# Kernel optimization log

Measured on AMD Instinct MI355X. Metric: run time of the kernel, lower is better.

Reference implementation:

```python
import jax, jax.numpy as jnp
import numpy as np
from jax import lax

SCORE_THRESH = 0.05
NMS_THRESH = 0.5
DET_PER_IMG = 100
K_PRE = 2048  # pre-NMS candidate cap (batched_nms is never run on N*C dense candidates)
BBOX_XFORM_CLIP = float(np.log(1000.0 / 16.0))
WX, WY, WW, WH = 10.0, 10.0, 5.0, 5.0


def _decode(reg, props):
    # reg: [N, C, 4] deltas, props: [N, 4] xyxy -> [N, C, 4] xyxy (torchvision BoxCoder.decode)
    w = props[:, 2] - props[:, 0]
    h = props[:, 3] - props[:, 1]
    cx = props[:, 0] + 0.5 * w
    cy = props[:, 1] + 0.5 * h
    dx = reg[..., 0] / WX
    dy = reg[..., 1] / WY
    dw = jnp.minimum(reg[..., 2] / WW, BBOX_XFORM_CLIP)
    dh = jnp.minimum(reg[..., 3] / WH, BBOX_XFORM_CLIP)
    pcx = dx * w[:, None] + cx[:, None]
    pcy = dy * h[:, None] + cy[:, None]
    pw = jnp.exp(dw) * w[:, None]
    ph = jnp.exp(dh) * h[:, None]
    return jnp.stack([pcx - 0.5 * pw, pcy - 0.5 * ph, pcx + 0.5 * pw, pcy + 0.5 * ph], axis=-1)


def _pairwise_iou(b):
    # b: [K, 4] -> [K, K]
    area = (b[:, 2] - b[:, 0]) * (b[:, 3] - b[:, 1])
    lt = jnp.maximum(b[:, None, :2], b[None, :, :2])
    rb = jnp.minimum(b[:, None, 2:], b[None, :, 2:])
    wh = jnp.clip(rb - lt, 0.0)
    inter = wh[..., 0] * wh[..., 1]
    return inter / (area[:, None] + area[None, :] - inter)


def _greedy_nms(iou, valid, thresh):
    # boxes assumed sorted by descending score; valid: [K] bool initial keep mask
    K = iou.shape[0]
    idx = jnp.arange(K)
    def body(i, keep):
        sup = (iou[i] > thresh) & (idx > i) & keep[i]
        return keep & (~sup)
    return lax.fori_loop(0, K, body, valid)


def _process_image(logits, reg, props, img_h, img_w):
    # logits: [N, C], reg: [N, 4C], props: [N, 4]
    N, C = logits.shape
    scores = jax.nn.softmax(logits, axis=-1)[:, 1:]          # [N, C-1] drop background
    boxes = _decode(reg.reshape(N, C, 4), props)[:, 1:]      # [N, C-1, 4]
    boxes = jnp.stack([
        jnp.clip(boxes[..., 0], 0.0, img_w),
        jnp.clip(boxes[..., 1], 0.0, img_h),
        jnp.clip(boxes[..., 2], 0.0, img_w),
        jnp.clip(boxes[..., 3], 0.0, img_h),
    ], axis=-1)
    labels = jnp.broadcast_to(jnp.arange(1, C), (N, C - 1))
    boxes = boxes.reshape(-1, 4)       # [M, 4], M = N*(C-1)
    scores = scores.reshape(-1)
    labels = labels.reshape(-1)
    wd = boxes[:, 2] - boxes[:, 0]
    ht = boxes[:, 3] - boxes[:, 1]
    valid = (scores > SCORE_THRESH) & (wd >= 1.0) & (ht >= 1.0)  # score thresh + remove_small_boxes
    masked = jnp.where(valid, scores, -1.0)
    top_s, top_i = lax.top_k(masked, K_PRE)
    tb = boxes[top_i]
    tl = labels[top_i]
    tvalid = top_s > SCORE_THRESH
    # batched_nms via per-class coordinate offsets
    off = tl.astype(tb.dtype) * (jnp.max(tb) + 1.0)
    keep = _greedy_nms(_pairwise_iou(tb + off[:, None]), tvalid, NMS_THRESH)
    ks = jnp.where(keep, top_s, -1.0)
    fs, fi = lax.top_k(ks, DET_PER_IMG)
    fvalid = fs > SCORE_THRESH
    out_boxes = jnp.where(fvalid[:, None], tb[fi], 0.0)
    out_scores = jnp.where(fvalid, fs, 0.0)
    out_labels = jnp.where(fvalid, tl[fi], -1)
    return out_boxes, out_scores, out_labels


def setup_inputs() -> dict:
    key = jax.random.key(0)
    k1, k2, k3 = jax.random.split(key, 3)
    B, N, C, H, W = 8, 4000, 91, 800, 800
    pts = jax.random.uniform(k1, (B, N, 2, 2), dtype=jnp.float32, minval=0.0, maxval=float(W))
    proposals = jnp.concatenate([pts.min(axis=2), pts.max(axis=2)], axis=-1)  # valid xyxy
    class_logits = jax.random.normal(k2, (B * N, C), dtype=jnp.float32)
    box_regression = 0.5 * jax.random.normal(k3, (B * N, 4 * C), dtype=jnp.float32)
    return {"class_logits": class_logits, "box_regression": box_regression,
            "proposals": proposals, "img_h": H, "img_w": W}


def reference(class_logits, box_regression, proposals, img_h, img_w):
    B, N, _ = proposals.shape
    C = class_logits.shape[-1]
    logits = class_logits.reshape(B, N, C)
    reg = box_regression.reshape(B, N, 4 * C)
    fn = lambda l, r, p: _process_image(l, r, p, float(img_h), float(img_w))
    boxes, scores, labels = jax.vmap(fn)(logits, reg, proposals)
    return boxes, scores, labels
```

## Files before the change

kernel.cpp:

```cpp
#include <hip/hip_runtime.h>
#include <stdint.h>

typedef unsigned int u32;
typedef unsigned long long u64;
typedef __attribute__((ext_vector_type(2))) unsigned long long u64x2;

#define BIMG 8
#define NPROP 4000
#define NCLS 91
#define CM1 90
#define MCAND (NPROP * CM1)
#define KPRE 2048
#define NBUCKET 4096
#define NREP 8
#define SELCAP 16384
#define DETS 100
#define WLCAP 2048
#define SCORE_T 0.05f
#define NMS_T 0.5f
#define BBOX_CLIP 4.135166556742356f

#define HISTREP_OFF ((size_t)0)
#define BCNTREP_OFF (HISTREP_OFF + (size_t)NREP * BIMG * NBUCKET * 4)
#define META_OFF    (BCNTREP_OFF + (size_t)NREP * BIMG * NBUCKET * 4)
#define ZERO_BYTES  (META_OFF + 4096)
#define START_OFF   (ZERO_BYTES)
#define HISTTOT_OFF (START_OFF + (size_t)BIMG * NBUCKET * 4)
#define STARTREP_OFF (HISTTOT_OFF + (size_t)BIMG * NBUCKET * 4)
#define SEL_OFF     (STARTREP_OFF + (size_t)NREP * BIMG * NBUCKET * 4)
#define TBOX_OFF    (SEL_OFF + (size_t)BIMG * SELCAP * 8)
#define TSB_OFF     (TBOX_OFF + (size_t)BIMG * KPRE * 16)
#define TSC_OFF     (TSB_OFF + (size_t)BIMG * KPRE * 16)
#define TLB_OFF     (TSC_OFF + (size_t)BIMG * KPRE * 4)
#define TVL_OFF     (TLB_OFF + (size_t)BIMG * KPRE * 4)
#define KEEP_OFF    (TVL_OFF + (size_t)BIMG * KPRE * 4)
#define WLIST_OFF   (KEEP_OFF + (size_t)BIMG * 32 * 8)
#define UNION_OFF   (WLIST_OFF + (size_t)BIMG * WLCAP * 4)
#define UNION_BYTES ((size_t)BIMG * MCAND * 4)
#define MASK_BYTES  ((size_t)BIMG * KPRE * 32 * 8)
#define WS_NEED     (UNION_OFF + UNION_BYTES)

__device__ __forceinline__ void decode_clip(const float4 rg, const float w, const float h,
                                            const float cx, const float cy,
                                            const float fw, const float fh, float bx[4]) {
    float dx = rg.x / 10.0f;
    float dy = rg.y / 10.0f;
    float dw = fminf(rg.z / 5.0f, BBOX_CLIP);
    float dh = fminf(rg.w / 5.0f, BBOX_CLIP);
    float pcx = dx * w + cx;
    float pcy = dy * h + cy;
    float pw  = expf(dw) * w;
    float phh = expf(dh) * h;
    bx[0] = fminf(fmaxf(pcx - 0.5f * pw,  0.0f), fw);
    bx[1] = fminf(fmaxf(pcy - 0.5f * phh, 0.0f), fh);
    bx[2] = fminf(fmaxf(pcx + 0.5f * pw,  0.0f), fw);
    bx[3] = fminf(fmaxf(pcy + 0.5f * phh, 0.0f), fh);
}

__global__ __launch_bounds__(256) void k1_score_hist(
    const float* __restrict__ logits, const float* __restrict__ reg,
    const float* __restrict__ props, const int* __restrict__ imh, const int* __restrict__ imw,
    u32* __restrict__ histrep, u32* __restrict__ cand_ord) {
    const int lane = threadIdx.x & 63;
    const int pid = blockIdx.x * 4 + (threadIdx.x >> 6);
    if (pid >= BIMG * NPROP) return;
    const int img = pid / NPROP;
    const float fw = (float)imw[0], fh = (float)imh[0];
    const float* lrow = logits + (size_t)pid * NCLS;
    float v0 = lrow[lane];
    float v1 = (lane < 27) ? lrow[lane + 64] : -3.0e38f;
    float mx = fmaxf(v0, v1);
#pragma unroll
    for (int o = 32; o > 0; o >>= 1) mx = fmaxf(mx, __shfl_xor(mx, o));
    float es = expf(v0 - mx) + ((lane < 27) ? expf(v1 - mx) : 0.0f);
#pragma unroll
    for (int o = 32; o > 0; o >>= 1) es += __shfl_xor(es, o);
    const float thr = mx + logf(es) - 2.9967323f;
    float4 p = reinterpret_cast<const float4*>(props)[pid];
    const float w = p.z - p.x, h = p.w - p.y;
    const float cx = p.x + 0.5f * w, cy = p.y + 0.5f * h;
    const float4* rrow = reinterpret_cast<const float4*>(reg) + (size_t)pid * NCLS;
    const int n = pid - img * NPROP;
    u32* co = cand_ord + (size_t)img * MCAND + (size_t)n * CM1;
#pragma unroll
    for (int batch = 0; batch < 2; ++batch) {
        int ci = lane + batch * 64;
        if (ci < CM1) {
            int c = ci + 1;
            float l = lrow[c];
            u32 o = 0u;
            if (l > thr) {
                float sc = expf(l - mx) / es;
                float4 rg = rrow[c];
                float bx[4];
                decode_clip(rg, w, h, cx, cy, fw, fh, bx);
                bool valid = (sc > SCORE_T) && (bx[2] - bx[0] >= 1.0f) && (bx[3] - bx[1] >= 1.0f);
                if (valid) {
                    o = __float_as_uint(sc) | 0x80000000u;
                    u32 t = (u32)img * MCAND + (u32)n * CM1 + (u32)ci;
                    int rep = (int)((t >> 8) & (NREP - 1));
                    atomicAdd(&histrep[((size_t)rep * BIMG + img) * NBUCKET + (o >> 20)], 1u);
                }
            }
            co[ci] = o;
        }
    }
}

__global__ __launch_bounds__(256) void k2_scan(
    const u32* __restrict__ histrep, u32* __restrict__ histtot,
    u32* __restrict__ start, u32* __restrict__ startrep, u32* __restrict__ meta,
    u32* __restrict__ wlist) {
    const int img = blockIdx.x;
    const int td = threadIdx.x;
    const int lane = td & 63, wv = td >> 6;
    u32 cnt[16]; u32 tsum = 0;
#pragma unroll
    for (int k = 0; k < 16; ++k) {
        const int bk = NBUCKET - 1 - (td * 16 + k);
        u32 c = 0;
#pragma unroll
        for (int r = 0; r < NREP; ++r)
            c += histrep[((size_t)r * BIMG + img) * NBUCKET + bk];
        cnt[k] = c; tsum += c;
    }
    u32 inc = tsum;
#pragma unroll
    for (int o = 1; o < 64; o <<= 1) { u32 t = __shfl_up(inc, o); if (lane >= o) inc += t; }
    __shared__ u32 wsum[4];
    __shared__ u32 TbkS, Vs;
    if (td == 0) TbkS = 0u;
    if (lane == 63) wsum[wv] = inc;
    __syncthreads();
    u32 wbase = 0;
    for (int i = 0; i < wv; ++i) wbase += wsum[i];
    if (td == 255) Vs = wbase + inc;
    const u32 excl0 = wbase + inc - tsum;
    u32 excl = excl0;
#pragma unroll
    for (int k = 0; k < 16; ++k) {
        const int bk = NBUCKET - 1 - (td * 16 + k);
        const u32 c = cnt[k];
        start[img * NBUCKET + bk] = excl;
        histtot[img * NBUCKET + bk] = c;
        u32 sub = excl;
#pragma unroll
        for (int r = 0; r < NREP; ++r) {
            startrep[((size_t)r * BIMG + img) * NBUCKET + bk] = sub;
            sub += histrep[((size_t)r * BIMG + img) * NBUCKET + bk];
        }
        if (c > 0 && excl < KPRE && excl + c >= KPRE) TbkS = (u32)bk;
        excl += c;
    }
    u32 qcnt = 0;
    {
        u32 e = excl0;
#pragma unroll
        for (int k = 0; k < 16; ++k) {
            if (cnt[k] >= 2 && e < KPRE) ++qcnt;
            e += cnt[k];
        }
    }
    u32 qinc = qcnt;
#pragma unroll
    for (int o = 1; o < 64; o <<= 1) { u32 t = __shfl_up(qinc, o); if (lane >= o) qinc += t; }
    __shared__ u32 qws[4];
    if (lane == 63) qws[wv] = qinc;
    __syncthreads();
    u32 qbase = 0;
    for (int i = 0; i < wv; ++i) qbase += qws[i];
    u32 qoff = qbase + qinc - qcnt;
    {
        u32 e = excl0;
#pragma unroll
        for (int k = 0; k < 16; ++k) {
            const int bk = NBUCKET - 1 - (td * 16 + k);
            if (cnt[k] >= 2 && e < KPRE && qoff < WLCAP) wlist[img * WLCAP + (qoff++)] = (u32)bk;
            e += cnt[k];
        }
    }
    if (td == 255) meta[img * 8 + 3] = qbase + qinc;
    __syncthreads();
    if (td == 0) {
        u32 V = Vs;
        meta[img * 8 + 0] = V;
        meta[img * 8 + 1] = TbkS;
        meta[img * 8 + 2] = (V < KPRE) ? (KPRE - V) : 0u;
    }
}

__global__ __launch_bounds__(256) void k3_compact(
    const u32* __restrict__ cand_ord, const u32* __restrict__ startrep,
    const u32* __restrict__ meta, u32* __restrict__ bcntrep, u64* __restrict__ sel) {
    const u32 t = blockIdx.x * 256 + threadIdx.x;
    const int rep = (int)(blockIdx.x & (NREP - 1));
    if (t >= (u32)(BIMG * MCAND)) return;
    const int img = t / MCAND;
    const u32 idx = t - (u32)img * MCAND;
    const u32 o = cand_ord[t];
    if (!o) return;
    const u32 bk = o >> 20;
    if (bk < meta[img * 8 + 1]) return;
    const size_t ri = ((size_t)rep * BIMG + img) * NBUCKET + bk;
    const u32 pos = startrep[ri] + atomicAdd(&bcntrep[ri], 1u);
    if (pos < SELCAP)
        sel[(size_t)img * SELCAP + pos] = ((u64)o << 32) | (u32)(~idx);
}

__global__ __launch_bounds__(64) void k3b_fill(
    const u32* __restrict__ cand_ord, const u32* __restrict__ meta, u64* __restrict__ sel) {
    const int img = blockIdx.x;
    const u32 need = meta[img * 8 + 2];
    if (need == 0) return;
    const u32 V = meta[img * 8 + 0];
    const int lane = threadIdx.x;
    const u32 ORDN1 = 0x407FFFFFu;
    u32 filled = 0;
    for (u32 b0 = 0; b0 < MCAND && filled < need; b0 += 64) {
        u32 idx = b0 + lane;
        bool inv = (idx < MCAND) && (cand_ord[(size_t)img * MCAND + idx] == 0u);
        u64 bal = __ballot(inv);
        u32 pre = (u32)__popcll(bal & ((1ull << lane) - 1ull));
        if (inv && (filled + pre) < need)
            sel[(size_t)img * SELCAP + V + filled + pre] = ((u64)ORDN1 << 32) | (u32)(~idx);
        filled += (u32)__popcll(bal);
    }
}

__global__ __launch_bounds__(256) void k4_sortseg(
    const u32* __restrict__ histtot, const u32* __restrict__ start,
    const u32* __restrict__ meta, const u32* __restrict__ wlist, u64* __restrict__ sel) {
    __shared__ u64 arr[4096];
    const int img = blockIdx.y;
    const int tid = threadIdx.x;
    const u32 wcount = meta[img * 8 + 3];
    for (u32 wi = blockIdx.x; wi < wcount; wi += gridDim.x) {
        const u32 bk = (wi < WLCAP) ? wlist[img * WLCAP + wi] : 0u;
        u32 cnt = histtot[img * NBUCKET + bk];
        u32 st = start[img * NBUCKET + bk];
        if (cnt < 2 || st >= KPRE) continue;
        if (st + cnt > SELCAP) cnt = SELCAP - st;
        if (cnt > 4096) cnt = 4096;
        int n = 1;
        while (n < (int)cnt) n <<= 1;
        u64* seg = sel + (size_t)img * SELCAP + st;
        for (int i = tid; i < n; i += 256) arr[i] = (i < (int)cnt) ? seg[i] : 0ull;
        __syncthreads();
        for (int k = 2; k <= n; k <<= 1)
            for (int j = k >> 1; j > 0; j >>= 1) {
                for (int i = tid; i < n; i += 256) {
                    int ixj = i ^ j;
                    if (ixj > i) {
                        u64 a = arr[i], b = arr[ixj];
                        bool swp = ((i & k) == 0) ? (a < b) : (a > b);
                        if (swp) { arr[i] = b; arr[ixj] = a; }
                    }
                }
                __syncthreads();
            }
        for (int i = tid; i < (int)cnt; i += 256) seg[i] = arr[i];
        __syncthreads();
    }
}

__global__ __launch_bounds__(256) void k5_gather(
    const u64* __restrict__ sel, const float* __restrict__ reg, const float* __restrict__ props,
    const int* __restrict__ imh, const int* __restrict__ imw,
    float* __restrict__ tbox, float* __restrict__ tsb, float* __restrict__ tsc,
    int* __restrict__ tlb, u32* __restrict__ tvl) {
    const int img = blockIdx.x;
    const int tid = threadIdx.x;
    const float fw = (float)imw[0], fh = (float)imh[0];
    float bx[8][4];
    int lab[8];
    float lm = -3.0e38f;
#pragma unroll
    for (int t = 0; t < 8; ++t) {
        int s = t * 256 + tid;
        u64 key = sel[(size_t)img * SELCAP + s];
        u32 o = (u32)(key >> 32);
        u32 idx = ~((u32)key);
        u32 b = (o & 0x80000000u) ? (o & 0x7FFFFFFFu) : ~o;
        float sc = __uint_as_float(b);
        u32 n = idx / CM1;
        int c = (int)(idx - n * CM1) + 1;
        int pid = img * NPROP + (int)n;
        float4 p = reinterpret_cast<const float4*>(props)[pid];
        float w = p.z - p.x, h = p.w - p.y;
        float cx = p.x + 0.5f * w, cy = p.y + 0.5f * h;
        float4 rg = reinterpret_cast<const float4*>(reg)[(size_t)pid * NCLS + c];
        decode_clip(rg, w, h, cx, cy, fw, fh, bx[t]);
        lab[t] = c;
        lm = fmaxf(lm, fmaxf(fmaxf(bx[t][0], bx[t][1]), fmaxf(bx[t][2], bx[t][3])));
        reinterpret_cast<float4*>(tbox)[(size_t)img * KPRE + s] =
            make_float4(bx[t][0], bx[t][1], bx[t][2], bx[t][3]);
        tsc[(size_t)img * KPRE + s] = sc;
        tlb[(size_t)img * KPRE + s] = c;
        tvl[(size_t)img * KPRE + s] = (sc > SCORE_T) ? 1u : 0u;
    }
#pragma unroll
    for (int o2 = 32; o2 > 0; o2 >>= 1) lm = fmaxf(lm, __shfl_xor(lm, o2));
    __shared__ float wm[4];
    if ((tid & 63) == 0) wm[tid >> 6] = lm;
    __syncthreads();
    float mplus = fmaxf(fmaxf(wm[0], wm[1]), fmaxf(wm[2], wm[3])) + 1.0f;
#pragma unroll
    for (int t = 0; t < 8; ++t) {
        int s = t * 256 + tid;
        float off = (float)lab[t] * mplus;
        reinterpret_cast<float4*>(tsb)[(size_t)img * KPRE + s] =
            make_float4(bx[t][0] + off, bx[t][1] + off, bx[t][2] + off, bx[t][3] + off);
    }
}

__global__ __launch_bounds__(64) void k6_mask(
    const float* __restrict__ tsb, u64* __restrict__ mask) {
    if (blockIdx.x < blockIdx.y) return;
    const int img = blockIdx.z;
    const int j0 = blockIdx.x * 64;
    const int i0 = blockIdx.y * 64;
    const int tid = threadIdx.x;
    __shared__ float4 cb[64];
    __shared__ float ca[64];
    float4 c = reinterpret_cast<const float4*>(tsb)[(size_t)img * KPRE + j0 + tid];
    cb[tid] = c;
    ca[tid] = (c.z - c.x) * (c.w - c.y);
    __syncthreads();
    const int i = i0 + tid;
    float4 r = reinterpret_cast<const float4*>(tsb)[(size_t)img * KPRE + i];
    float ra = (r.z - r.x) * (r.w - r.y);
    u64 bits = 0ull;
#pragma unroll 8
    for (int jj = 0; jj < 64; ++jj) {
        int j = j0 + jj;
        float4 cc = cb[jj];
        float wv = fmaxf(fminf(r.z, cc.z) - fmaxf(r.x, cc.x), 0.0f);
        float hv = fmaxf(fminf(r.w, cc.w) - fmaxf(r.y, cc.y), 0.0f);
        float inter = wv * hv;
        float iou = inter / ((ra + ca[jj]) - inter);
        if ((iou > NMS_T) && (j > i)) bits |= (1ull << jj);
    }
    mask[((size_t)img * KPRE + i) * 32 + (j0 >> 6)] = bits;
}

__device__ __forceinline__ u64 rdlane64(u64 v, int l) {
    u32 lo = (u32)__builtin_amdgcn_readlane((int)(u32)v, l);
    u32 hi = (u32)__builtin_amdgcn_readlane((int)(u32)(v >> 32), l);
    return ((u64)hi << 32) | lo;
}

__device__ __forceinline__ void g2l16(const void* g, void* l) {
    __builtin_amdgcn_global_load_lds(
        (const __attribute__((address_space(1))) void*)g,
        (__attribute__((address_space(3))) void*)l, 16, 0, 0);
}

__global__ __launch_bounds__(64) void k7_nms(
    const u64* __restrict__ mask, const u32* __restrict__ tvl, u64* __restrict__ keepw) {
    __shared__ u64 lbuf[2][2048];
    const int img = blockIdx.x;
    const int lane = threadIdx.x;
    const int lg = lane >> 4;
    const u64* mrow = mask + (size_t)img * KPRE * 32;

    u64 accx = 0ull, accy = 0ull, rp = 0ull;
    for (int w = 0; w < 32; ++w) {
        bool tv = tvl[(size_t)img * KPRE + w * 64 + lane] != 0u;
        u64 iw = ~__ballot(tv);
        if (w == 0) rp = iw;
        if ((lane & 15) == (w >> 1)) { if (w & 1) accy = iw; else accx = iw; }
    }

    {
        const char* gsrc = (const char*)mrow + (size_t)lane * 16;
#pragma unroll
        for (int t = 0; t < 16; ++t)
            g2l16(gsrc + (size_t)t * 1024, (char*)&lbuf[0][0] + (size_t)t * 1024);
    }
    u64 diag = mrow[(size_t)lane * 32];

    u32 tk = 0;
    int bcut = 31;

#pragma unroll 1
    for (int b = 0; b < 32; ++b) {
        const size_t base32 = (size_t)b * 2048;
        const u64* cbuf = &lbuf[b & 1][0];

        u64 diagn = 0ull;
        if (b + 1 < 32) {
            diagn = mrow[base32 + 2048 + (size_t)lane * 32 + (b + 1)];
            const char* gsrc = (const char*)(mrow + base32 + 2048) + (size_t)lane * 16;
            char* nb_l = (char*)&lbuf[(b + 1) & 1][0];
#pragma unroll
            for (int t = 0; t < 16; ++t)
                g2l16(gsrc + (size_t)t * 1024, nb_l + (size_t)t * 1024);
        }

        u64 A = rp;
#pragma unroll
        for (int u = 0; u < 64; ++u) {
            u64 row = rdlane64(diag, u);
            if (!((A >> u) & 1ull)) A |= row;
        }
        const u64 keptw = ~A;

        if (b + 1 < 32) asm volatile("s_waitcnt vmcnt(17)" ::: "memory");
        else            asm volatile("s_waitcnt vmcnt(0)" ::: "memory");

#define LDV(K) u64x2 v##K = *(const u64x2*)&cbuf[128 * (K) + 2 * lane];
#define PRV(K) { u32 nib = (u32)(keptw >> (4 * (K))) & 15u; \
                 u32 kb = (nib >> lg) & 1u; \
                 accx |= kb ? v##K.x : 0ull; accy |= kb ? v##K.y : 0ull; }
        LDV(0) LDV(1) LDV(2) LDV(3)
        LDV(4) LDV(5) LDV(6) LDV(7)     PRV(0) PRV(1) PRV(2) PRV(3)
        LDV(8) LDV(9) LDV(10) LDV(11)   PRV(4) PRV(5) PRV(6) PRV(7)
        LDV(12) LDV(13) LDV(14) LDV(15) PRV(8) PRV(9) PRV(10) PRV(11)
        PRV(12) PRV(13) PRV(14) PRV(15)
#undef LDV
#undef PRV

        tk += (u32)__popcll(keptw);
        if (tk >= (u32)DETS) { bcut = b; break; }

        const int nb2 = b + 1;
        if (nb2 < 32) {
            u64 asel = (nb2 & 1) ? accy : accx;
            const int sl = (nb2 >> 1) & 15;
            rp = rdlane64(asel, sl) | rdlane64(asel, sl + 16) |
                 rdlane64(asel, sl + 32) | rdlane64(asel, sl + 48);
        }
        diag = diagn;
    }

    asm volatile("s_waitcnt vmcnt(0)" ::: "memory");

    accx |= __shfl_xor(accx, 16); accx |= __shfl_xor(accx, 32);
    accy |= __shfl_xor(accy, 16); accy |= __shfl_xor(accy, 32);
    if (lane < 16) {
        keepw[img * 32 + 2 * lane]     = (2 * lane     <= bcut) ? ~accx : 0ull;
        keepw[img * 32 + 2 * lane + 1] = (2 * lane + 1 <= bcut) ? ~accy : 0ull;
    }
}

__global__ __launch_bounds__(64) void k8_select(
    const u64* __restrict__ keepw, const float* __restrict__ tsc,
    const float* __restrict__ tbox, const int* __restrict__ tlb,
    float* __restrict__ out) {
    const int img = blockIdx.x;
    const int lane = threadIdx.x;
    u64 kw = (lane < 32) ? keepw[img * 32 + lane] : 0ull;
    u32 cnt = (u32)__popcll(kw);
    u32 inc = cnt;
#pragma unroll
    for (int o = 1; o < 64; o <<= 1) { u32 t = __shfl_up(inc, o); if (lane >= o) inc += t; }
    const u32 excl = inc - cnt;
    const u32 total = (u32)__shfl(inc, 63);

    float* ob0 = out + (size_t)img * DETS * 4;
    float* os0 = out + (size_t)BIMG * DETS * 4 + (size_t)img * DETS;
    float* ol0 = out + (size_t)BIMG * DETS * 5 + (size_t)img * DETS;

#pragma unroll
    for (int t = 0; t < 2; ++t) {
        u32 r = (u32)lane + (u32)t * 64;
        if (r < DETS && r >= total) {
            reinterpret_cast<float4*>(ob0)[r] = make_float4(0.f, 0.f, 0.f, 0.f);
            os0[r] = 0.0f;
            ol0[r] = -1.0f;
        }
    }

    u64 w = kw;
    u32 r = excl;
    while (w != 0ull && r < DETS) {
        int p = __ffsll((unsigned long long)w) - 1;
        w &= (w - 1ull);
        u32 s = (u32)lane * 64u + (u32)p;
        reinterpret_cast<float4*>(ob0)[r] =
            reinterpret_cast<const float4*>(tbox)[(size_t)img * KPRE + s];
        os0[r] = tsc[(size_t)img * KPRE + s];
        ol0[r] = (float)tlb[(size_t)img * KPRE + s];
        ++r;
    }
}

extern "C" void kernel_launch(void* const* d_in, const int* in_sizes, int n_in,
                              void* d_out, int out_size, void* d_ws, size_t ws_size,
                              hipStream_t stream) {
    const float* logits = (const float*)d_in[0];
    const float* reg    = (const float*)d_in[1];
    const float* props  = (const float*)d_in[2];
    const int*   imh    = (const int*)d_in[3];
    const int*   imw    = (const int*)d_in[4];
    float* out = (float*)d_out;
    char* ws = (char*)d_ws;
    if (ws_size < WS_NEED) return;

    u32* histrep  = (u32*)(ws + HISTREP_OFF);
    u32* bcntrep  = (u32*)(ws + BCNTREP_OFF);
    u32* meta     = (u32*)(ws + META_OFF);
    u32* start    = (u32*)(ws + START_OFF);
    u32* histtot  = (u32*)(ws + HISTTOT_OFF);
    u32* startrep = (u32*)(ws + STARTREP_OFF);
    u64* sel  = (u64*)(ws + SEL_OFF);
    float* tbox = (float*)(ws + TBOX_OFF);
    float* tsb  = (float*)(ws + TSB_OFF);
    float* tsc  = (float*)(ws + TSC_OFF);
    int*   tlb  = (int*)(ws + TLB_OFF);
    u32*   tvl  = (u32*)(ws + TVL_OFF);
    u64*   keepw = (u64*)(ws + KEEP_OFF);
    u32*   wlist = (u32*)(ws + WLIST_OFF);
    u32*   cand_ord = (u32*)(ws + UNION_OFF);
    u64*   mask = (u64*)(ws + UNION_OFF);

    hipMemsetAsync(d_ws, 0, ZERO_BYTES, stream);

    k1_score_hist<<<BIMG * NPROP / 4, 256, 0, stream>>>(logits, reg, props, imh, imw,
                                                        histrep, cand_ord);
    k2_scan<<<BIMG, 256, 0, stream>>>(histrep, histtot, start, startrep, meta, wlist);
    k3_compact<<<(BIMG * MCAND) / 256, 256, 0, stream>>>(cand_ord, startrep, meta, bcntrep, sel);
    k3b_fill<<<BIMG, 64, 0, stream>>>(cand_ord, meta, sel);
    hipMemsetAsync(mask, 0, MASK_BYTES, stream);
    k4_sortseg<<<dim3(64, BIMG), 256, 0, stream>>>(histtot, start, meta, wlist, sel);
    k5_gather<<<BIMG, 256, 0, stream>>>(sel, reg, props, imh, imw, tbox, tsb, tsc, tlb, tvl);
    k6_mask<<<dim3(32, 32, BIMG), 64, 0, stream>>>(tsb, mask);
    k7_nms<<<BIMG, 64, 0, stream>>>(mask, tvl, keepw);
    k8_select<<<BIMG, 64, 0, stream>>>(keepw, tsc, tbox, tlb, out);
}
```

Baseline: 272.8 us.

## Fuse all pipeline stages into one cooperative persistent kernel with grid syncs

Replaces the ten separate launches (two memsets plus eight kernels) with a single cooperative kernel of 256 blocks. Stages are separated by grid.sync(), workspace zeroing moves into the kernel, and the NMS and selection stages are merged so the keep words never round-trip through memory. This aims to remove per-launch overhead and inter-kernel gaps. In exchange, stages that used many blocks now run with a fixed 65536 threads, and each grid barrier has its own cost.

New measurement: 494.4 us. 81.3% more time.

```diff
diff --git a/kernel.cpp b/kernel.cpp
--- a/kernel.cpp
+++ b/kernel.cpp
@@ -1,5 +1,8 @@
 #include <hip/hip_runtime.h>
+#include <hip/hip_cooperative_groups.h>
 #include <stdint.h>
+
+namespace cg = cooperative_groups;
 
 typedef unsigned int u32;
 typedef unsigned long long u64;
@@ -37,8 +40,11 @@
 #define WLIST_OFF   (KEEP_OFF + (size_t)BIMG * 32 * 8)
 #define UNION_OFF   (WLIST_OFF + (size_t)BIMG * WLCAP * 4)
 #define UNION_BYTES ((size_t)BIMG * MCAND * 4)
-#define MASK_BYTES  ((size_t)BIMG * KPRE * 32 * 8)
 #define WS_NEED     (UNION_OFF + UNION_BYTES)
+
+#define ZW ((u32)(ZERO_BYTES / 4))
+#define MW ((u32)(BIMG * KPRE * 32))
+#define NTHREADS 65536
 
 __device__ __forceinline__ void decode_clip(const float4 rg, const float w, const float h,
                                             const float cx, const float cy,
@@ -57,292 +63,6 @@
     bx[3] = fminf(fmaxf(pcy + 0.5f * phh, 0.0f), fh);
 }
 
-__global__ __launch_bounds__(256) void k1_score_hist(
-    const float* __restrict__ logits, const float* __restrict__ reg,
-    const float* __restrict__ props, const int* __restrict__ imh, const int* __restrict__ imw,
-    u32* __restrict__ histrep, u32* __restrict__ cand_ord) {
-    const int lane = threadIdx.x & 63;
-    const int pid = blockIdx.x * 4 + (threadIdx.x >> 6);
-    if (pid >= BIMG * NPROP) return;
-    const int img = pid / NPROP;
-    const float fw = (float)imw[0], fh = (float)imh[0];
-    const float* lrow = logits + (size_t)pid * NCLS;
-    float v0 = lrow[lane];
-    float v1 = (lane < 27) ? lrow[lane + 64] : -3.0e38f;
-    float mx = fmaxf(v0, v1);
-#pragma unroll
-    for (int o = 32; o > 0; o >>= 1) mx = fmaxf(mx, __shfl_xor(mx, o));
-    float es = expf(v0 - mx) + ((lane < 27) ? expf(v1 - mx) : 0.0f);
-#pragma unroll
-    for (int o = 32; o > 0; o >>= 1) es += __shfl_xor(es, o);
-    const float thr = mx + logf(es) - 2.9967323f;
-    float4 p = reinterpret_cast<const float4*>(props)[pid];
-    const float w = p.z - p.x, h = p.w - p.y;
-    const float cx = p.x + 0.5f * w, cy = p.y + 0.5f * h;
-    const float4* rrow = reinterpret_cast<const float4*>(reg) + (size_t)pid * NCLS;
-    const int n = pid - img * NPROP;
-    u32* co = cand_ord + (size_t)img * MCAND + (size_t)n * CM1;
-#pragma unroll
-    for (int batch = 0; batch < 2; ++batch) {
-        int ci = lane + batch * 64;
-        if (ci < CM1) {
-            int c = ci + 1;
-            float l = lrow[c];
-            u32 o = 0u;
-            if (l > thr) {
-                float sc = expf(l - mx) / es;
-                float4 rg = rrow[c];
-                float bx[4];
-                decode_clip(rg, w, h, cx, cy, fw, fh, bx);
-                bool valid = (sc > SCORE_T) && (bx[2] - bx[0] >= 1.0f) && (bx[3] - bx[1] >= 1.0f);
-                if (valid) {
-                    o = __float_as_uint(sc) | 0x80000000u;
-                    u32 t = (u32)img * MCAND + (u32)n * CM1 + (u32)ci;
-                    int rep = (int)((t >> 8) & (NREP - 1));
-                    atomicAdd(&histrep[((size_t)rep * BIMG + img) * NBUCKET + (o >> 20)], 1u);
-                }
-            }
-            co[ci] = o;
-        }
-    }
-}
-
-__global__ __launch_bounds__(256) void k2_scan(
-    const u32* __restrict__ histrep, u32* __restrict__ histtot,
-    u32* __restrict__ start, u32* __restrict__ startrep, u32* __restrict__ meta,
-    u32* __restrict__ wlist) {
-    const int img = blockIdx.x;
-    const int td = threadIdx.x;
-    const int lane = td & 63, wv = td >> 6;
-    u32 cnt[16]; u32 tsum = 0;
-#pragma unroll
-    for (int k = 0; k < 16; ++k) {
-        const int bk = NBUCKET - 1 - (td * 16 + k);
-        u32 c = 0;
-#pragma unroll
-        for (int r = 0; r < NREP; ++r)
-            c += histrep[((size_t)r * BIMG + img) * NBUCKET + bk];
-        cnt[k] = c; tsum += c;
-    }
-    u32 inc = tsum;
-#pragma unroll
-    for (int o = 1; o < 64; o <<= 1) { u32 t = __shfl_up(inc, o); if (lane >= o) inc += t; }
-    __shared__ u32 wsum[4];
-    __shared__ u32 TbkS, Vs;
-    if (td == 0) TbkS = 0u;
-    if (lane == 63) wsum[wv] = inc;
-    __syncthreads();
-    u32 wbase = 0;
-    for (int i = 0; i < wv; ++i) wbase += wsum[i];
-    if (td == 255) Vs = wbase + inc;
-    const u32 excl0 = wbase + inc - tsum;
-    u32 excl = excl0;
-#pragma unroll
-    for (int k = 0; k < 16; ++k) {
-        const int bk = NBUCKET - 1 - (td * 16 + k);
-        const u32 c = cnt[k];
-        start[img * NBUCKET + bk] = excl;
-        histtot[img * NBUCKET + bk] = c;
-        u32 sub = excl;
-#pragma unroll
-        for (int r = 0; r < NREP; ++r) {
-            startrep[((size_t)r * BIMG + img) * NBUCKET + bk] = sub;
-            sub += histrep[((size_t)r * BIMG + img) * NBUCKET + bk];
-        }
-        if (c > 0 && excl < KPRE && excl + c >= KPRE) TbkS = (u32)bk;
-        excl += c;
-    }
-    u32 qcnt = 0;
-    {
-        u32 e = excl0;
-#pragma unroll
-        for (int k = 0; k < 16; ++k) {
-            if (cnt[k] >= 2 && e < KPRE) ++qcnt;
-            e += cnt[k];
-        }
-    }
-    u32 qinc = qcnt;
-#pragma unroll
-    for (int o = 1; o < 64; o <<= 1) { u32 t = __shfl_up(qinc, o); if (lane >= o) qinc += t; }
-    __shared__ u32 qws[4];
-    if (lane == 63) qws[wv] = qinc;
-    __syncthreads();
-    u32 qbase = 0;
-    for (int i = 0; i < wv; ++i) qbase += qws[i];
-    u32 qoff = qbase + qinc - qcnt;
-    {
-        u32 e = excl0;
-#pragma unroll
-        for (int k = 0; k < 16; ++k) {
-            const int bk = NBUCKET - 1 - (td * 16 + k);
-            if (cnt[k] >= 2 && e < KPRE && qoff < WLCAP) wlist[img * WLCAP + (qoff++)] = (u32)bk;
-            e += cnt[k];
-        }
-    }
-    if (td == 255) meta[img * 8 + 3] = qbase + qinc;
-    __syncthreads();
-    if (td == 0) {
-        u32 V = Vs;
-        meta[img * 8 + 0] = V;
-        meta[img * 8 + 1] = TbkS;
-        meta[img * 8 + 2] = (V < KPRE) ? (KPRE - V) : 0u;
-    }
-}
-
-__global__ __launch_bounds__(256) void k3_compact(
-    const u32* __restrict__ cand_ord, const u32* __restrict__ startrep,
-    const u32* __restrict__ meta, u32* __restrict__ bcntrep, u64* __restrict__ sel) {
-    const u32 t = blockIdx.x * 256 + threadIdx.x;
-    const int rep = (int)(blockIdx.x & (NREP - 1));
-    if (t >= (u32)(BIMG * MCAND)) return;
-    const int img = t / MCAND;
-    const u32 idx = t - (u32)img * MCAND;
-    const u32 o = cand_ord[t];
-    if (!o) return;
-    const u32 bk = o >> 20;
-    if (bk < meta[img * 8 + 1]) return;
-    const size_t ri = ((size_t)rep * BIMG + img) * NBUCKET + bk;
-    const u32 pos = startrep[ri] + atomicAdd(&bcntrep[ri], 1u);
-    if (pos < SELCAP)
-        sel[(size_t)img * SELCAP + pos] = ((u64)o << 32) | (u32)(~idx);
-}
-
-__global__ __launch_bounds__(64) void k3b_fill(
-    const u32* __restrict__ cand_ord, const u32* __restrict__ meta, u64* __restrict__ sel) {
-    const int img = blockIdx.x;
-    const u32 need = meta[img * 8 + 2];
-    if (need == 0) return;
-    const u32 V = meta[img * 8 + 0];
-    const int lane = threadIdx.x;
-    const u32 ORDN1 = 0x407FFFFFu;
-    u32 filled = 0;
-    for (u32 b0 = 0; b0 < MCAND && filled < need; b0 += 64) {
-        u32 idx = b0 + lane;
-        bool inv = (idx < MCAND) && (cand_ord[(size_t)img * MCAND + idx] == 0u);
-        u64 bal = __ballot(inv);
-        u32 pre = (u32)__popcll(bal & ((1ull << lane) - 1ull));
-        if (inv && (filled + pre) < need)
-            sel[(size_t)img * SELCAP + V + filled + pre] = ((u64)ORDN1 << 32) | (u32)(~idx);
-        filled += (u32)__popcll(bal);
-    }
-}
-
-__global__ __launch_bounds__(256) void k4_sortseg(
-    const u32* __restrict__ histtot, const u32* __restrict__ start,
-    const u32* __restrict__ meta, const u32* __restrict__ wlist, u64* __restrict__ sel) {
-    __shared__ u64 arr[4096];
-    const int img = blockIdx.y;
-    const int tid = threadIdx.x;
-    const u32 wcount = meta[img * 8 + 3];
-    for (u32 wi = blockIdx.x; wi < wcount; wi += gridDim.x) {
-        const u32 bk = (wi < WLCAP) ? wlist[img * WLCAP + wi] : 0u;
-        u32 cnt = histtot[img * NBUCKET + bk];
-        u32 st = start[img * NBUCKET + bk];
-        if (cnt < 2 || st >= KPRE) continue;
-        if (st + cnt > SELCAP) cnt = SELCAP - st;
-        if (cnt > 4096) cnt = 4096;
-        int n = 1;
-        while (n < (int)cnt) n <<= 1;
-        u64* seg = sel + (size_t)img * SELCAP + st;
-        for (int i = tid; i < n; i += 256) arr[i] = (i < (int)cnt) ? seg[i] : 0ull;
-        __syncthreads();
-        for (int k = 2; k <= n; k <<= 1)
-            for (int j = k >> 1; j > 0; j >>= 1) {
-                for (int i = tid; i < n; i += 256) {
-                    int ixj = i ^ j;
-                    if (ixj > i) {
-                        u64 a = arr[i], b = arr[ixj];
-                        bool swp = ((i & k) == 0) ? (a < b) : (a > b);
-                        if (swp) { arr[i] = b; arr[ixj] = a; }
-                    }
-                }
-                __syncthreads();
-            }
-        for (int i = tid; i < (int)cnt; i += 256) seg[i] = arr[i];
-        __syncthreads();
-    }
-}
-
-__global__ __launch_bounds__(256) void k5_gather(
-    const u64* __restrict__ sel, const float* __restrict__ reg, const float* __restrict__ props,
-    const int* __restrict__ imh, const int* __restrict__ imw,
-    float* __restrict__ tbox, float* __restrict__ tsb, float* __restrict__ tsc,
-    int* __restrict__ tlb, u32* __restrict__ tvl) {
-    const int img = blockIdx.x;
-    const int tid = threadIdx.x;
-    const float fw = (float)imw[0], fh = (float)imh[0];
-    float bx[8][4];
-    int lab[8];
-    float lm = -3.0e38f;
-#pragma unroll
-    for (int t = 0; t < 8; ++t) {
-        int s = t * 256 + tid;
-        u64 key = sel[(size_t)img * SELCAP + s];
-        u32 o = (u32)(key >> 32);
-        u32 idx = ~((u32)key);
-        u32 b = (o & 0x80000000u) ? (o & 0x7FFFFFFFu) : ~o;
-        float sc = __uint_as_float(b);
-        u32 n = idx / CM1;
-        int c = (int)(idx - n * CM1) + 1;
-        int pid = img * NPROP + (int)n;
-        float4 p = reinterpret_cast<const float4*>(props)[pid];
-        float w = p.z - p.x, h = p.w - p.y;
-        float cx = p.x + 0.5f * w, cy = p.y + 0.5f * h;
-        float4 rg = reinterpret_cast<const float4*>(reg)[(size_t)pid * NCLS + c];
-        decode_clip(rg, w, h, cx, cy, fw, fh, bx[t]);
-        lab[t] = c;
-        lm = fmaxf(lm, fmaxf(fmaxf(bx[t][0], bx[t][1]), fmaxf(bx[t][2], bx[t][3])));
-        reinterpret_cast<float4*>(tbox)[(size_t)img * KPRE + s] =
-            make_float4(bx[t][0], bx[t][1], bx[t][2], bx[t][3]);
-        tsc[(size_t)img * KPRE + s] = sc;
-        tlb[(size_t)img * KPRE + s] = c;
-        tvl[(size_t)img * KPRE + s] = (sc > SCORE_T) ? 1u : 0u;
-    }
-#pragma unroll
-    for (int o2 = 32; o2 > 0; o2 >>= 1) lm = fmaxf(lm, __shfl_xor(lm, o2));
-    __shared__ float wm[4];
-    if ((tid & 63) == 0) wm[tid >> 6] = lm;
-    __syncthreads();
-    float mplus = fmaxf(fmaxf(wm[0], wm[1]), fmaxf(wm[2], wm[3])) + 1.0f;
-#pragma unroll
-    for (int t = 0; t < 8; ++t) {
-        int s = t * 256 + tid;
-        float off = (float)lab[t] * mplus;
-        reinterpret_cast<float4*>(tsb)[(size_t)img * KPRE + s] =
-            make_float4(bx[t][0] + off, bx[t][1] + off, bx[t][2] + off, bx[t][3] + off);
-    }
-}
-
-__global__ __launch_bounds__(64) void k6_mask(
-    const float* __restrict__ tsb, u64* __restrict__ mask) {
-    if (blockIdx.x < blockIdx.y) return;
-    const int img = blockIdx.z;
-    const int j0 = blockIdx.x * 64;
-    const int i0 = blockIdx.y * 64;
-    const int tid = threadIdx.x;
-    __shared__ float4 cb[64];
-    __shared__ float ca[64];
-    float4 c = reinterpret_cast<const float4*>(tsb)[(size_t)img * KPRE + j0 + tid];
-    cb[tid] = c;
-    ca[tid] = (c.z - c.x) * (c.w - c.y);
-    __syncthreads();
-    const int i = i0 + tid;
-    float4 r = reinterpret_cast<const float4*>(tsb)[(size_t)img * KPRE + i];
-    float ra = (r.z - r.x) * (r.w - r.y);
-    u64 bits = 0ull;
-#pragma unroll 8
-    for (int jj = 0; jj < 64; ++jj) {
-        int j = j0 + jj;
-        float4 cc = cb[jj];
-        float wv = fmaxf(fminf(r.z, cc.z) - fmaxf(r.x, cc.x), 0.0f);
-        float hv = fmaxf(fminf(r.w, cc.w) - fmaxf(r.y, cc.y), 0.0f);
-        float inter = wv * hv;
-        float iou = inter / ((ra + ca[jj]) - inter);
-        if ((iou > NMS_T) && (j > i)) bits |= (1ull << jj);
-    }
-    mask[((size_t)img * KPRE + i) * 32 + (j0 >> 6)] = bits;
-}
-
 __device__ __forceinline__ u64 rdlane64(u64 v, int l) {
     u32 lo = (u32)__builtin_amdgcn_readlane((int)(u32)v, l);
     u32 hi = (u32)__builtin_amdgcn_readlane((int)(u32)(v >> 32), l);
@@ -355,133 +75,419 @@
         (__attribute__((address_space(3))) void*)l, 16, 0, 0);
 }
 
-__global__ __launch_bounds__(64) void k7_nms(
-    const u64* __restrict__ mask, const u32* __restrict__ tvl, u64* __restrict__ keepw) {
-    __shared__ u64 lbuf[2][2048];
-    const int img = blockIdx.x;
-    const int lane = threadIdx.x;
-    const int lg = lane >> 4;
-    const u64* mrow = mask + (size_t)img * KPRE * 32;
-
-    u64 accx = 0ull, accy = 0ull, rp = 0ull;
-    for (int w = 0; w < 32; ++w) {
-        bool tv = tvl[(size_t)img * KPRE + w * 64 + lane] != 0u;
-        u64 iw = ~__ballot(tv);
-        if (w == 0) rp = iw;
-        if ((lane & 15) == (w >> 1)) { if (w & 1) accy = iw; else accx = iw; }
-    }
+__global__ __launch_bounds__(256) void mega(
+    const float* __restrict__ logits, const float* __restrict__ reg,
+    const float* __restrict__ props, const int* __restrict__ imh,
+    const int* __restrict__ imw,
+    u32* __restrict__ histrep, u32* __restrict__ bcntrep, u32* __restrict__ meta,
+    u32* __restrict__ start, u32* __restrict__ histtot, u32* __restrict__ startrep,
+    u64* __restrict__ sel, float* __restrict__ tbox, float* __restrict__ tsb,
+    float* __restrict__ tsc, int* __restrict__ tlb, u32* __restrict__ tvl,
+    u32* __restrict__ wlist, u32* cand_ord, u64* mask,
+    float* __restrict__ out) {
+    cg::grid_group grid = cg::this_grid();
+    __shared__ u64 smem[4096];
+    __shared__ u32 s_wsum[4], s_qws[4], s_TbkS, s_Vs;
+    __shared__ float s_wm[4];
+
+    const int tid = threadIdx.x;
+    const u32 gtid = blockIdx.x * 256u + (u32)tid;
+    const int lane = tid & 63;
+
+    for (u32 i = gtid; i < ZW; i += NTHREADS) histrep[i] = 0u;
+    grid.sync();
 
     {
-        const char* gsrc = (const char*)mrow + (size_t)lane * 16;
-#pragma unroll
-        for (int t = 0; t < 16; ++t)
-            g2l16(gsrc + (size_t)t * 1024, (char*)&lbuf[0][0] + (size_t)t * 1024);
-    }
-    u64 diag = mrow[(size_t)lane * 32];
-
-    u32 tk = 0;
-    int bcut = 31;
+        const int wid = (int)(gtid >> 6);
+        const float fw = (float)imw[0], fh = (float)imh[0];
+        for (int pid = wid; pid < BIMG * NPROP; pid += NTHREADS / 64) {
+            const int img = pid / NPROP;
+            const float* lrow = logits + (size_t)pid * NCLS;
+            float v0 = lrow[lane];
+            float v1 = (lane < 27) ? lrow[lane + 64] : -3.0e38f;
+            float mx = fmaxf(v0, v1);
+#pragma unroll
+            for (int o = 32; o > 0; o >>= 1) mx = fmaxf(mx, __shfl_xor(mx, o));
+            float es = expf(v0 - mx) + ((lane < 27) ? expf(v1 - mx) : 0.0f);
+#pragma unroll
+            for (int o = 32; o > 0; o >>= 1) es += __shfl_xor(es, o);
+            const float thr = mx + logf(es) - 2.9967323f;
+            float4 p = reinterpret_cast<const float4*>(props)[pid];
+            const float w = p.z - p.x, h = p.w - p.y;
+            const float cx = p.x + 0.5f * w, cy = p.y + 0.5f * h;
+            const float4* rrow = reinterpret_cast<const float4*>(reg) + (size_t)pid * NCLS;
+            const int n = pid - img * NPROP;
+            u32* co = cand_ord + (size_t)img * MCAND + (size_t)n * CM1;
+#pragma unroll
+            for (int batch = 0; batch < 2; ++batch) {
+                int ci = lane + batch * 64;
+                if (ci < CM1) {
+                    int c = ci + 1;
+                    float l = lrow[c];
+                    u32 o = 0u;
+                    if (l > thr) {
+                        float sc = expf(l - mx) / es;
+                        float4 rg = rrow[c];
+                        float bx[4];
+                        decode_clip(rg, w, h, cx, cy, fw, fh, bx);
+                        bool valid = (sc > SCORE_T) && (bx[2] - bx[0] >= 1.0f) &&
+                                     (bx[3] - bx[1] >= 1.0f);
+                        if (valid) {
+                            o = __float_as_uint(sc) | 0x80000000u;
+                            u32 t = (u32)img * MCAND + (u32)n * CM1 + (u32)ci;
+                            int rep = (int)((t >> 8) & (NREP - 1));
+                            atomicAdd(&histrep[((size_t)rep * BIMG + img) * NBUCKET + (o >> 20)], 1u);
+                        }
+                    }
+                    co[ci] = o;
+                }
+            }
+        }
+    }
+    grid.sync();
+
+    if (blockIdx.x < BIMG) {
+        const int img = blockIdx.x;
+        const int td = tid;
+        const int wv = td >> 6;
+        u32 cnt[16]; u32 tsum = 0;
+#pragma unroll
+        for (int k = 0; k < 16; ++k) {
+            const int bk = NBUCKET - 1 - (td * 16 + k);
+            u32 c = 0;
+#pragma unroll
+            for (int r = 0; r < NREP; ++r)
+                c += histrep[((size_t)r * BIMG + img) * NBUCKET + bk];
+            cnt[k] = c; tsum += c;
+        }
+        u32 inc = tsum;
+#pragma unroll
+        for (int o = 1; o < 64; o <<= 1) { u32 t = __shfl_up(inc, o); if (lane >= o) inc += t; }
+        if (td == 0) s_TbkS = 0u;
+        if (lane == 63) s_wsum[wv] = inc;
+        __syncthreads();
+        u32 wbase = 0;
+        for (int i = 0; i < wv; ++i) wbase += s_wsum[i];
+        if (td == 255) s_Vs = wbase + inc;
+        const u32 excl0 = wbase + inc - tsum;
+        u32 excl = excl0;
+#pragma unroll
+        for (int k = 0; k < 16; ++k) {
+            const int bk = NBUCKET - 1 - (td * 16 + k);
+            const u32 c = cnt[k];
+            start[img * NBUCKET + bk] = excl;
+            histtot[img * NBUCKET + bk] = c;
+            u32 sub = excl;
+#pragma unroll
+            for (int r = 0; r < NREP; ++r) {
+                startrep[((size_t)r * BIMG + img) * NBUCKET + bk] = sub;
+                sub += histrep[((size_t)r * BIMG + img) * NBUCKET + bk];
+            }
+            if (c > 0 && excl < KPRE && excl + c >= KPRE) s_TbkS = (u32)bk;
+            excl += c;
+        }
+        u32 qcnt = 0;
+        {
+            u32 e = excl0;
+#pragma unroll
+            for (int k = 0; k < 16; ++k) { if (cnt[k] >= 2 && e < KPRE) ++qcnt; e += cnt[k]; }
+        }
+        u32 qinc = qcnt;
+#pragma unroll
+        for (int o = 1; o < 64; o <<= 1) { u32 t = __shfl_up(qinc, o); if (lane >= o) qinc += t; }
+        if (lane == 63) s_qws[wv] = qinc;
+        __syncthreads();
+        u32 qbase = 0;
+        for (int i = 0; i < wv; ++i) qbase += s_qws[i];
+        u32 qoff = qbase + qinc - qcnt;
+        {
+            u32 e = excl0;
+#pragma unroll
+            for (int k = 0; k < 16; ++k) {
+                const int bk = NBUCKET - 1 - (td * 16 + k);
+                if (cnt[k] >= 2 && e < KPRE && qoff < WLCAP) wlist[img * WLCAP + (qoff++)] = (u32)bk;
+                e += cnt[k];
+            }
+        }
+        if (td == 255) meta[img * 8 + 3] = qbase + qinc;
+        __syncthreads();
+        if (td == 0) {
+            u32 V = s_Vs;
+            meta[img * 8 + 0] = V;
+            meta[img * 8 + 1] = s_TbkS;
+            meta[img * 8 + 2] = (V < KPRE) ? (KPRE - V) : 0u;
+        }
+    }
+    grid.sync();
+
+    {
+        const u32 TOT = (u32)BIMG * (u32)MCAND;
+        for (u32 t = gtid; t < TOT; t += NTHREADS) {
+            const u32 o = cand_ord[t];
+            if (!o) continue;
+            const int img = (int)(t / (u32)MCAND);
+            const u32 idx = t - (u32)img * (u32)MCAND;
+            const u32 bk = o >> 20;
+            if (bk < meta[img * 8 + 1]) continue;
+            const int rep = (int)((t >> 8) & (NREP - 1));
+            const size_t ri = ((size_t)rep * BIMG + img) * NBUCKET + bk;
+            const u32 pos = startrep[ri] + atomicAdd(&bcntrep[ri], 1u);
+            if (pos < SELCAP)
+                sel[(size_t)img * SELCAP + pos] = ((u64)o << 32) | (u32)(~idx);
+        }
+        if (blockIdx.x < BIMG && tid < 64) {
+            const int img = blockIdx.x;
+            const u32 need = meta[img * 8 + 2];
+            if (need != 0) {
+                const u32 V = meta[img * 8 + 0];
+                const u32 ORDN1 = 0x407FFFFFu;
+                u32 filled = 0;
+                for (u32 b0 = 0; b0 < MCAND && filled < need; b0 += 64) {
+                    u32 idx = b0 + (u32)lane;
+                    bool inv = (idx < MCAND) && (cand_ord[(size_t)img * MCAND + idx] == 0u);
+                    u64 bal = __ballot(inv);
+                    u32 pre = (u32)__popcll(bal & ((1ull << lane) - 1ull));
+                    if (inv && (filled + pre) < need)
+                        sel[(size_t)img * SELCAP + V + filled + pre] =
+                            ((u64)ORDN1 << 32) | (u32)(~idx);
+                    filled += (u32)__popcll(bal);
+                }
+            }
+        }
+    }
+    grid.sync();
+
+    {
+        for (u32 i = gtid; i < MW; i += NTHREADS) mask[i] = 0ull;
+
+        const int img = blockIdx.x & 7;
+        const u32 wcount = meta[img * 8 + 3];
+        u64* arr = smem;
+        for (u32 wi = (u32)(blockIdx.x >> 3); wi < wcount; wi += 32) {
+            const u32 bk = (wi < WLCAP) ? wlist[img * WLCAP + wi] : 0u;
+            u32 cnt = histtot[img * NBUCKET + bk];
+            u32 st = start[img * NBUCKET + bk];
+            if (cnt < 2 || st >= KPRE) continue;
+            if (st + cnt > SELCAP) cnt = SELCAP - st;
+            if (cnt > 4096) cnt = 4096;
+            int n = 1;
+            while (n < (int)cnt) n <<= 1;
+            u64* seg = sel + (size_t)img * SELCAP + st;
+            for (int i = tid; i < n; i += 256) arr[i] = (i < (int)cnt) ? seg[i] : 0ull;
+            __syncthreads();
+            for (int k = 2; k <= n; k <<= 1)
+                for (int j = k >> 1; j > 0; j >>= 1) {
+                    for (int i = tid; i < n; i += 256) {
+                        int ixj = i ^ j;
+                        if (ixj > i) {
+                            u64 a = arr[i], b = arr[ixj];
+                            bool swp = ((i & k) == 0) ? (a < b) : (a > b);
+                            if (swp) { arr[i] = b; arr[ixj] = a; }
+                        }
+                    }
+                    __syncthreads();
+                }
+            for (int i = tid; i < (int)cnt; i += 256) seg[i] = arr[i];
+            __syncthreads();
+        }
+    }
+    grid.sync();
+
+    if (blockIdx.x < BIMG) {
+        const int img = blockIdx.x;
+        const float fw = (float)imw[0], fh = (float)imh[0];
+        float bx[8][4];
+        int lab[8];
+        float lm = -3.0e38f;
+#pragma unroll
+        for (int t = 0; t < 8; ++t) {
+            int s = t * 256 + tid;
+            u64 key = sel[(size_t)img * SELCAP + s];
+            u32 o = (u32)(key >> 32);
+            u32 idx = ~((u32)key);
+            u32 b = (o & 0x80000000u) ? (o & 0x7FFFFFFFu) : ~o;
+            float sc = __uint_as_float(b);
+            u32 n = idx / CM1;
+            int c = (int)(idx - n * CM1) + 1;
+            int pid = img * NPROP + (int)n;
+            float4 p = reinterpret_cast<const float4*>(props)[pid];
+            float w = p.z - p.x, h = p.w - p.y;
+            float cx = p.x + 0.5f * w, cy = p.y + 0.5f * h;
+            float4 rg = reinterpret_cast<const float4*>(reg)[(size_t)pid * NCLS + c];
+            decode_clip(rg, w, h, cx, cy, fw, fh, bx[t]);
+            lab[t] = c;
+            lm = fmaxf(lm, fmaxf(fmaxf(bx[t][0], bx[t][1]), fmaxf(bx[t][2], bx[t][3])));
+            reinterpret_cast<float4*>(tbox)[(size_t)img * KPRE + s] =
+                make_float4(bx[t][0], bx[t][1], bx[t][2], bx[t][3]);
+            tsc[(size_t)img * KPRE + s] = sc;
+            tlb[(size_t)img * KPRE + s] = c;
+            tvl[(size_t)img * KPRE + s] = (sc > SCORE_T) ? 1u : 0u;
+        }
+#pragma unroll
+        for (int o2 = 32; o2 > 0; o2 >>= 1) lm = fmaxf(lm, __shfl_xor(lm, o2));
+        if (lane == 0) s_wm[tid >> 6] = lm;
+        __syncthreads();
+        float mplus = fmaxf(fmaxf(s_wm[0], s_wm[1]), fmaxf(s_wm[2], s_wm[3])) + 1.0f;
+#pragma unroll
+        for (int t = 0; t < 8; ++t) {
+            int s = t * 256 + tid;
+            float off = (float)lab[t] * mplus;
+            reinterpret_cast<float4*>(tsb)[(size_t)img * KPRE + s] =
+                make_float4(bx[t][0] + off, bx[t][1] + off, bx[t][2] + off, bx[t][3] + off);
+        }
+    }
+    grid.sync();
+
+    {
+        const int wid = (int)(gtid >> 6);
+        for (int T = wid; T < BIMG * 528; T += NTHREADS / 64) {
+            const int img = T / 528;
+            int rem = T - img * 528;
+            int by = 0;
+            while (rem >= 32 - by) { rem -= (32 - by); ++by; }
+            const int bx_ = by + rem;
+            const int i0 = by * 64, j0 = bx_ * 64;
+            const float4* tsb4 = reinterpret_cast<const float4*>(tsb) + (size_t)img * KPRE;
+            float4 c = tsb4[j0 + lane];
+            float cao = (c.z - c.x) * (c.w - c.y);
+            float4 r = tsb4[i0 + lane];
+            float ra = (r.z - r.x) * (r.w - r.y);
+            const int i = i0 + lane;
+            u64 bits = 0ull;
+#pragma unroll 8
+            for (int jj = 0; jj < 64; ++jj) {
+                float ccx = __shfl(c.x, jj), ccy = __shfl(c.y, jj);
+                float ccz = __shfl(c.z, jj), ccw = __shfl(c.w, jj);
+                float caj = __shfl(cao, jj);
+                float wv = fmaxf(fminf(r.z, ccz) - fmaxf(r.x, ccx), 0.0f);
+                float hv = fmaxf(fminf(r.w, ccw) - fmaxf(r.y, ccy), 0.0f);
+                float inter = wv * hv;
+                float iou = inter / ((ra + caj) - inter);
+                int j = j0 + jj;
+                if ((iou > NMS_T) && (j > i)) bits |= (1ull << jj);
+            }
+            mask[((size_t)img * KPRE + i) * 32 + (j0 >> 6)] = bits;
+        }
+    }
+    grid.sync();
+
+    if (blockIdx.x < BIMG && tid < 64) {
+        const int img = blockIdx.x;
+        const int lg = lane >> 4;
+        const u64* mrow = mask + (size_t)img * KPRE * 32;
+
+        u64 accx = 0ull, accy = 0ull, rp = 0ull;
+        for (int w = 0; w < 32; ++w) {
+            bool tv = tvl[(size_t)img * KPRE + w * 64 + lane] != 0u;
+            u64 iw = ~__ballot(tv);
+            if (w == 0) rp = iw;
+            if ((lane & 15) == (w >> 1)) { if (w & 1) accy = iw; else accx = iw; }
+        }
+
+        {
+            const char* gsrc = (const char*)mrow + (size_t)lane * 16;
+#pragma unroll
+            for (int t = 0; t < 16; ++t)
+                g2l16(gsrc + (size_t)t * 1024, (char*)smem + (size_t)t * 1024);
+        }
+        u64 diag = mrow[(size_t)lane * 32];
+
+        u32 tk = 0;
+        int bcut = 31;
 
 #pragma unroll 1
-    for (int b = 0; b < 32; ++b) {
-        const size_t base32 = (size_t)b * 2048;
-        const u64* cbuf = &lbuf[b & 1][0];
-
-        u64 diagn = 0ull;
-        if (b + 1 < 32) {
-            diagn = mrow[base32 + 2048 + (size_t)lane * 32 + (b + 1)];
-            const char* gsrc = (const char*)(mrow + base32 + 2048) + (size_t)lane * 16;
-            char* nb_l = (char*)&lbuf[(b + 1) & 1][0];
-#pragma unroll
-            for (int t = 0; t < 16; ++t)
-                g2l16(gsrc + (size_t)t * 1024, nb_l + (size_t)t * 1024);
-        }
-
-        u64 A = rp;
-#pragma unroll
-        for (int u = 0; u < 64; ++u) {
-            u64 row = rdlane64(diag, u);
-            if (!((A >> u) & 1ull)) A |= row;
-        }
-        const u64 keptw = ~A;
-
-        if (b + 1 < 32) asm volatile("s_waitcnt vmcnt(17)" ::: "memory");
-        else            asm volatile("s_waitcnt vmcnt(0)" ::: "memory");
+        for (int b = 0; b < 32; ++b) {
+            const size_t base32 = (size_t)b * 2048;
+            const u64* cbuf = smem + (size_t)(b & 1) * 2048;
+
+            u64 diagn = 0ull;
+            if (b + 1 < 32) {
+                diagn = mrow[base32 + 2048 + (size_t)lane * 32 + (b + 1)];
+                const char* gsrc = (const char*)(mrow + base32 + 2048) + (size_t)lane * 16;
+                char* nb_l = (char*)(smem + (size_t)((b + 1) & 1) * 2048);
+#pragma unroll
+                for (int t = 0; t < 16; ++t)
+                    g2l16(gsrc + (size_t)t * 1024, nb_l + (size_t)t * 1024);
+            }
+
+            u64 A = rp;
+#pragma unroll
+            for (int u = 0; u < 64; ++u) {
+                u64 row = rdlane64(diag, u);
+                if (!((A >> u) & 1ull)) A |= row;
+            }
+            const u64 keptw = ~A;
+
+            if (b + 1 < 32) asm volatile("s_waitcnt vmcnt(17)" ::: "memory");
+            else            asm volatile("s_waitcnt vmcnt(0)" ::: "memory");
 
 #define LDV(K) u64x2 v##K = *(const u64x2*)&cbuf[128 * (K) + 2 * lane];
 #define PRV(K) { u32 nib = (u32)(keptw >> (4 * (K))) & 15u; \
                  u32 kb = (nib >> lg) & 1u; \
                  accx |= kb ? v##K.x : 0ull; accy |= kb ? v##K.y : 0ull; }
-        LDV(0) LDV(1) LDV(2) LDV(3)
-        LDV(4) LDV(5) LDV(6) LDV(7)     PRV(0) PRV(1) PRV(2) PRV(3)
-        LDV(8) LDV(9) LDV(10) LDV(11)   PRV(4) PRV(5) PRV(6) PRV(7)
-        LDV(12) LDV(13) LDV(14) LDV(15) PRV(8) PRV(9) PRV(10) PRV(11)
-        PRV(12) PRV(13) PRV(14) PRV(15)
+            LDV(0) LDV(1) LDV(2) LDV(3)
+            LDV(4) LDV(5) LDV(6) LDV(7)     PRV(0) PRV(1) PRV(2) PRV(3)
+            LDV(8) LDV(9) LDV(10) LDV(11)   PRV(4) PRV(5) PRV(6) PRV(7)
+            LDV(12) LDV(13) LDV(14) LDV(15) PRV(8) PRV(9) PRV(10) PRV(11)
+            PRV(12) PRV(13) PRV(14) PRV(15)
 #undef LDV
 #undef PRV
 
-        tk += (u32)__popcll(keptw);
-        if (tk >= (u32)DETS) { bcut = b; break; }
-
-        const int nb2 = b + 1;
-        if (nb2 < 32) {
-            u64 asel = (nb2 & 1) ? accy : accx;
-            const int sl = (nb2 >> 1) & 15;
-            rp = rdlane64(asel, sl) | rdlane64(asel, sl + 16) |
-                 rdlane64(asel, sl + 32) | rdlane64(asel, sl + 48);
-        }
-        diag = diagn;
-    }
-
-    asm volatile("s_waitcnt vmcnt(0)" ::: "memory");
-
-    accx |= __shfl_xor(accx, 16); accx |= __shfl_xor(accx, 32);
-    accy |= __shfl_xor(accy, 16); accy |= __shfl_xor(accy, 32);
-    if (lane < 16) {
-        keepw[img * 32 + 2 * lane]     = (2 * lane     <= bcut) ? ~accx : 0ull;
-        keepw[img * 32 + 2 * lane + 1] = (2 * lane + 1 <= bcut) ? ~accy : 0ull;
-    }
-}
-
-__global__ __launch_bounds__(64) void k8_select(
-    const u64* __restrict__ keepw, const float* __restrict__ tsc,
-    const float* __restrict__ tbox, const int* __restrict__ tlb,
-    float* __restrict__ out) {
-    const int img = blockIdx.x;
-    const int lane = threadIdx.x;
-    u64 kw = (lane < 32) ? keepw[img * 32 + lane] : 0ull;
-    u32 cnt = (u32)__popcll(kw);
-    u32 inc = cnt;
-#pragma unroll
-    for (int o = 1; o < 64; o <<= 1) { u32 t = __shfl_up(inc, o); if (lane >= o) inc += t; }
-    const u32 excl = inc - cnt;
-    const u32 total = (u32)__shfl(inc, 63);
-
-    float* ob0 = out + (size_t)img * DETS * 4;
-    float* os0 = out + (size_t)BIMG * DETS * 4 + (size_t)img * DETS;
-    float* ol0 = out + (size_t)BIMG * DETS * 5 + (size_t)img * DETS;
-
-#pragma unroll
-    for (int t = 0; t < 2; ++t) {
-        u32 r = (u32)lane + (u32)t * 64;
-        if (r < DETS && r >= total) {
-            reinterpret_cast<float4*>(ob0)[r] = make_float4(0.f, 0.f, 0.f, 0.f);
-            os0[r] = 0.0f;
-            ol0[r] = -1.0f;
-        }
-    }
-
-    u64 w = kw;
-    u32 r = excl;
-    while (w != 0ull && r < DETS) {
-        int p = __ffsll((unsigned long long)w) - 1;
-        w &= (w - 1ull);
-        u32 s = (u32)lane * 64u + (u32)p;
-        reinterpret_cast<float4*>(ob0)[r] =
-            reinterpret_cast<const float4*>(tbox)[(size_t)img * KPRE + s];
-        os0[r] = tsc[(size_t)img * KPRE + s];
-        ol0[r] = (float)tlb[(size_t)img * KPRE + s];
-        ++r;
+            tk += (u32)__popcll(keptw);
+            if (tk >= (u32)DETS) { bcut = b; break; }
+
+            const int nb2 = b + 1;
+            if (nb2 < 32) {
+                u64 asel = (nb2 & 1) ? accy : accx;
+                const int sl = (nb2 >> 1) & 15;
+                rp = rdlane64(asel, sl) | rdlane64(asel, sl + 16) |
+                     rdlane64(asel, sl + 32) | rdlane64(asel, sl + 48);
+            }
+            diag = diagn;
+        }
+
+        asm volatile("s_waitcnt vmcnt(0)" ::: "memory");
+
+        accx |= __shfl_xor(accx, 16); accx |= __shfl_xor(accx, 32);
+        accy |= __shfl_xor(accy, 16); accy |= __shfl_xor(accy, 32);
+
+        u64 mxv = __shfl(accx, (lane >> 1) & 15);
+        u64 myv = __shfl(accy, (lane >> 1) & 15);
+        u64 kw = (lane & 1) ? ~myv : ~mxv;
+        if (lane >= 32 || lane > bcut) kw = 0ull;
+
+        u32 cnt = (u32)__popcll(kw);
+        u32 inc = cnt;
+#pragma unroll
+        for (int o = 1; o < 64; o <<= 1) { u32 t = __shfl_up(inc, o); if (lane >= o) inc += t; }
+        const u32 excl = inc - cnt;
+        const u32 total = (u32)__shfl(inc, 63);
+
+        float* ob0 = out + (size_t)img * DETS * 4;
+        float* os0 = out + (size_t)BIMG * DETS * 4 + (size_t)img * DETS;
+        float* ol0 = out + (size_t)BIMG * DETS * 5 + (size_t)img * DETS;
+
+#pragma unroll
+        for (int t = 0; t < 2; ++t) {
+            u32 r = (u32)lane + (u32)t * 64;
+            if (r < DETS && r >= total) {
+                reinterpret_cast<float4*>(ob0)[r] = make_float4(0.f, 0.f, 0.f, 0.f);
+                os0[r] = 0.0f;
+                ol0[r] = -1.0f;
+            }
+        }
+        u64 w = kw;
+        u32 r = excl;
+        while (w != 0ull && r < DETS) {
+            int p = __ffsll((unsigned long long)w) - 1;
+            w &= (w - 1ull);
+            u32 s = (u32)lane * 64u + (u32)p;
+            reinterpret_cast<float4*>(ob0)[r] =
+                reinterpret_cast<const float4*>(tbox)[(size_t)img * KPRE + s];
+            os0[r] = tsc[(size_t)img * KPRE + s];
+            ol0[r] = (float)tlb[(size_t)img * KPRE + s];
+            ++r;
+        }
     }
 }
 
@@ -509,22 +515,16 @@
     float* tsc  = (float*)(ws + TSC_OFF);
     int*   tlb  = (int*)(ws + TLB_OFF);
     u32*   tvl  = (u32*)(ws + TVL_OFF);
-    u64*   keepw = (u64*)(ws + KEEP_OFF);
     u32*   wlist = (u32*)(ws + WLIST_OFF);
     u32*   cand_ord = (u32*)(ws + UNION_OFF);
     u64*   mask = (u64*)(ws + UNION_OFF);
 
-    hipMemsetAsync(d_ws, 0, ZERO_BYTES, stream);
-
-    k1_score_hist<<<BIMG * NPROP / 4, 256, 0, stream>>>(logits, reg, props, imh, imw,
-                                                        histrep, cand_ord);
-    k2_scan<<<BIMG, 256, 0, stream>>>(histrep, histtot, start, startrep, meta, wlist);
-    k3_compact<<<(BIMG * MCAND) / 256, 256, 0, stream>>>(cand_ord, startrep, meta, bcntrep, sel);
-    k3b_fill<<<BIMG, 64, 0, stream>>>(cand_ord, meta, sel);
-    hipMemsetAsync(mask, 0, MASK_BYTES, stream);
-    k4_sortseg<<<dim3(64, BIMG), 256, 0, stream>>>(histtot, start, meta, wlist, sel);
-    k5_gather<<<BIMG, 256, 0, stream>>>(sel, reg, props, imh, imw, tbox, tsb, tsc, tlb, tvl);
-    k6_mask<<<dim3(32, 32, BIMG), 64, 0, stream>>>(tsb, mask);
-    k7_nms<<<BIMG, 64, 0, stream>>>(mask, tvl, keepw);
-    k8_select<<<BIMG, 64, 0, stream>>>(keepw, tsc, tbox, tlb, out);
+    void* args[] = {
+        (void*)&logits, (void*)&reg, (void*)&props, (void*)&imh, (void*)&imw,
+        (void*)&histrep, (void*)&bcntrep, (void*)&meta, (void*)&start,
+        (void*)&histtot, (void*)&startrep, (void*)&sel, (void*)&tbox,
+        (void*)&tsb, (void*)&tsc, (void*)&tlb, (void*)&tvl, (void*)&wlist,
+        (void*)&cand_ord, (void*)&mask, (void*)&out
+    };
+    hipLaunchCooperativeKernel((const void*)mega, dim3(256), dim3(256), args, 0, stream);
 }
```
